# Performance work log

Measured on AMD Instinct MI355X. Metric: run time of the kernel, lower is better.

Reference implementation:

```python
import jax, jax.numpy as jnp
import numpy as np
import math

B_, L_, H_, N_ = 4, 4096, 512, 128

def setup_inputs() -> dict:
    key = jax.random.key(0)
    ks = jax.random.split(key, 6)
    return {
        "x": jax.random.normal(ks[0], (B_, L_, H_), dtype=jnp.float32),
        "log_Lam_real": jnp.log(0.5 * jnp.ones((N_,), jnp.float32)),  # log(-lam_real), lam_real=-0.5
        "Lam_imag": math.pi * jnp.arange(N_, dtype=jnp.float32),
        "B_real": jax.random.normal(ks[1], (N_, H_), jnp.float32) * 0.02,
        "B_imag": jax.random.normal(ks[2], (N_, H_), jnp.float32) * 0.02,
        "C_real": jax.random.normal(ks[3], (H_, N_), jnp.float32) * 0.02,
        "C_imag": jax.random.normal(ks[4], (H_, N_), jnp.float32) * 0.02,
        "D": jnp.ones((H_,), jnp.float32),
        "log_dt": jnp.zeros((1,), jnp.float32),
        "W_out": jax.random.normal(ks[5], (H_, H_), jnp.float32) * (1.0 / math.sqrt(H_)),
        "b_out": jnp.zeros((H_,), jnp.float32),
    }

def reference(x, log_Lam_real, Lam_imag, B_real, B_imag, C_real, C_imag, D, log_dt, W_out, b_out):
    B, L, H = x.shape
    N = log_Lam_real.shape[0]
    dt = jnp.exp(log_dt)                      # (1,)
    Lam_r = -jnp.exp(log_Lam_real)            # (N,)
    decay = jnp.exp(Lam_r * dt)               # (N,)
    Lbar_r = decay * jnp.cos(Lam_imag * dt)   # (N,)
    Lbar_i = decay * jnp.sin(Lam_imag * dt)   # (N,)
    # Precompute input projections for all timesteps: u @ (dt*B).T -> (B, L, N)
    Bu_r = dt * jnp.einsum('blh,nh->bln', x, B_real)
    Bu_i = dt * jnp.einsum('blh,nh->bln', x, B_imag)

    def step(carry, inp):
        sr, si = carry
        br, bi = inp
        sr_n = Lbar_r * sr - Lbar_i * si + br
        si_n = Lbar_r * si + Lbar_i * sr + bi
        return (sr_n, si_n), (sr_n, si_n)

    init = (jnp.zeros((B, N), x.dtype), jnp.zeros((B, N), x.dtype))
    (sr_f, si_f), (Sr, Si) = jax.lax.scan(
        step, init, (jnp.swapaxes(Bu_r, 0, 1), jnp.swapaxes(Bu_i, 0, 1)))
    Sr = jnp.swapaxes(Sr, 0, 1)  # (B, L, N)
    Si = jnp.swapaxes(Si, 0, 1)
    y = (jnp.einsum('bln,hn->blh', Sr, C_real)
         - jnp.einsum('bln,hn->blh', Si, C_imag)
         + D * x)
    out = y @ W_out.T + b_out  # dropout p=0 -> identity
    return out, (sr_f, si_f)
```

## Files before the change

kernel.cpp:

```cpp
#include <hip/hip_runtime.h>

typedef __attribute__((ext_vector_type(8))) short bf16x8;
typedef __attribute__((ext_vector_type(4))) float f32x4;

__device__ __forceinline__ unsigned short f2bf(float f) {
  unsigned u = __float_as_uint(f);
  return (unsigned short)((u + 0x7fffu + ((u >> 16) & 1u)) >> 16);
}
__device__ __forceinline__ float bf2f(unsigned short h) {
  return __uint_as_float(((unsigned)h) << 16);
}
__device__ __forceinline__ void gload_lds16(const void* g, void* l) {
  __builtin_amdgcn_global_load_lds((__attribute__((address_space(1))) void*)g,
                                   (__attribute__((address_space(3))) void*)l,
                                   16, 0, 0);
}
#define VMCNT(n) asm volatile("s_waitcnt vmcnt(" #n ")" ::: "memory")
#define LGKM0() asm volatile("s_waitcnt lgkmcnt(0)" ::: "memory")
#define SB0() __builtin_amdgcn_sched_barrier(0)
#define BAR() __builtin_amdgcn_s_barrier()

__global__ __launch_bounds__(256) void prepW1_k(
    const float* __restrict__ log_dt,
    const float* __restrict__ B_real, const float* __restrict__ B_imag,
    unsigned short* __restrict__ W1) {
  const float dtv = expf(log_dt[0]);
  const int i = blockIdx.x * 256 + threadIdx.x;
  const int j = i >> 9, h = i & 511;
  const float v = (j < 128) ? B_real[j * 512 + h] : B_imag[(j - 128) * 512 + h];
  W1[i] = f2bf(dtv * v);
}

__global__ __launch_bounds__(512, 1) void fused1_k(
    const float* __restrict__ x, const unsigned short* __restrict__ W1g,
    unsigned short* __restrict__ xbf, unsigned short* __restrict__ S2,
    const float* __restrict__ log_Lam_real, const float* __restrict__ Lam_imag,
    const float* __restrict__ log_dt, float* __restrict__ finals,
    const float* __restrict__ C_real, const float* __restrict__ C_imag,
    const float* __restrict__ W_out, const float* __restrict__ Dv,
    unsigned short* __restrict__ W45) {
  __shared__ unsigned short lds[61440];
  const int tid = threadIdx.x;
  const int bid = blockIdx.x;

  if (bid >= 256) {
    if (bid < 768) {
      const int i = (bid - 256) * 512 + tid;
      const int j = i >> 9, h = i & 511;
      W45[j * 768 + 256 + h] = f2bf(W_out[i] * Dv[h]);
    } else {
      float4* red = (float4*)lds;
      const int j0 = (bid - 768) * 2;
      const int kg = tid & 63;
      const int hc = tid >> 6;
      const int k4 = kg * 4;
      const bool im = (kg >= 32);
      const float* cbase = im ? (C_imag + (k4 - 128)) : (C_real + k4);
      const float* w0 = W_out + (long)j0 * 512;
      const float* w1 = w0 + 512;
      float4 acc0 = {0.f, 0.f, 0.f, 0.f}, acc1 = {0.f, 0.f, 0.f, 0.f};
#pragma unroll 8
      for (int hh = 0; hh < 64; ++hh) {
        const int h = hc * 64 + hh;
        const float4 cv = *(const float4*)(cbase + (long)h * 128);
        const float s0 = w0[h], s1 = w1[h];
        acc0.x += cv.x * s0; acc0.y += cv.y * s0; acc0.z += cv.z * s0; acc0.w += cv.w * s0;
        acc1.x += cv.x * s1; acc1.y += cv.y * s1; acc1.z += cv.z * s1; acc1.w += cv.w * s1;
      }
      if (im) {
        acc0.x = -acc0.x; acc0.y = -acc0.y; acc0.z = -acc0.z; acc0.w = -acc0.w;
        acc1.x = -acc1.x; acc1.y = -acc1.y; acc1.z = -acc1.z; acc1.w = -acc1.w;
      }
      red[(hc * 2 + 0) * 64 + kg] = acc0;
      red[(hc * 2 + 1) * 64 + kg] = acc1;
      __syncthreads();
      if (tid < 128) {
        const int r = tid >> 6, g = tid & 63;
        float4 s = {0.f, 0.f, 0.f, 0.f};
#pragma unroll
        for (int h8 = 0; h8 < 8; ++h8) {
          const float4 t = red[(h8 * 2 + r) * 64 + g];
          s.x += t.x; s.y += t.y; s.z += t.z; s.w += t.w;
        }
        unsigned short* o = W45 + (long)(j0 + r) * 768 + g * 4;
        o[0] = f2bf(s.x); o[1] = f2bf(s.y); o[2] = f2bf(s.z); o[3] = f2bf(s.w);
      }
    }
    return;
  }

  const int c = (bid & 7) * 32 + (bid >> 3);
  const int b = c >> 6, cb = c & 63;
  const int warm = cb ? 32 : 0;
  const long base = (long)b * 4096 + (long)cb * 64 - warm;

  const float dtv = expf(log_dt[0]);
  const int nidx = tid & 127;
  const float lamr = -expf(log_Lam_real[nidx]);
  const float dec = expf(lamr * dtv);
  const float th = Lam_imag[nidx] * dtv;
  const float Lr = dec * cosf(th);
  const float Li = dec * sinf(th);

  const int arow = tid >> 4;
  const int cg = tid & 15;
  const int wid_ = tid >> 6, lane_ = tid & 63;

  float4 a0S0, a1S0, a2S0, a0S1, a1S1, a2S1, a0S2, a1S2, a2S2;

#define LOADA(S, kt) {                                                   \
    const float* xp = x + base * 512 + (kt) * 64 + cg * 4;               \
    a0##S = *(const float4*)(xp + (long)arow * 512);                     \
    a1##S = *(const float4*)(xp + (long)(arow + 32) * 512);              \
    a2##S = *(const float4*)(xp + (long)(arow + 64) * 512); }

#define WRA1(V, R, buf, kt, DOX) {                                       \
    ushort4 hh_; hh_.x = f2bf(V.x); hh_.y = f2bf(V.y);                   \
    hh_.z = f2bf(V.z); hh_.w = f2bf(V.w);                                \
    const int seg_ = (cg >> 1) ^ ((R) & 7);                              \
    *(ushort4*)((char*)lds + (buf) * 12288 + (R) * 128 + seg_ * 16 +     \
                (cg & 1) * 8) = hh_;                                     \
    if (DOX) *(ushort4*)(xbf + (base + (R)) * 512 + (kt) * 64 + cg * 4) = hh_; }

#define WRITEA(S, buf, kt) {                                             \
    WRA1(a0##S, arow, buf, kt, (warm == 0));                             \
    WRA1(a1##S, arow + 32, buf, kt, 1);                                  \
    WRA1(a2##S, arow + 64, buf, kt, 1); }

  auto stageW = [&](int buf, int kt) {
#pragma unroll
    for (int i = 0; i < 4; ++i) {
      const int q = i * 8 + wid_;
      const int r = q * 8 + (lane_ >> 3);
      const int sg = lane_ & 7;
      gload_lds16(W1g + (long)r * 512 + kt * 64 + ((sg ^ (r & 7)) << 3),
                  lds + 12288 + buf * 16384 + q * 512 + lane_ * 8);
    }
  };

  const int wm = (wid_ >> 2) * 48;
  const int wn = (wid_ & 3) * 64;
  const int lrow = lane_ & 15, lgrp = lane_ >> 4;

  f32x4 acc[3][4];
#pragma unroll
  for (int mi = 0; mi < 3; ++mi)
#pragma unroll
    for (int ni = 0; ni < 4; ++ni) acc[mi][ni] = (f32x4){0.f, 0.f, 0.f, 0.f};

  auto mfma_step = [&](int abuf, int wbuf) {
    const unsigned short* As = lds + abuf * 6144;
    const unsigned short* Ws = lds + 12288 + wbuf * 16384;
#pragma unroll
    for (int kk = 0; kk < 2; ++kk) {
      bf16x8 af[3], wf[4];
#pragma unroll
      for (int mi = 0; mi < 3; ++mi) {
        const int r = wm + mi * 16 + lrow;
        af[mi] = *(const bf16x8*)(As + r * 64 + (((kk * 4 + lgrp) ^ (r & 7)) << 3));
      }
#pragma unroll
      for (int ni = 0; ni < 4; ++ni) {
        const int r = wn + ni * 16 + lrow;
        wf[ni] = *(const bf16x8*)(Ws + r * 64 + (((kk * 4 + lgrp) ^ (r & 7)) << 3));
      }
#pragma unroll
      for (int mi = 0; mi < 3; ++mi)
#pragma unroll
        for (int ni = 0; ni < 4; ++ni)
          acc[mi][ni] = __builtin_amdgcn_mfma_f32_16x16x32_bf16(af[mi], wf[ni],
                                                                acc[mi][ni], 0, 0, 0);
    }
  };

  LOADA(S0, 0);
  stageW(0, 0);
  VMCNT(4);
  WRITEA(S0, 0, 0);
  LOADA(S1, 1);
  stageW(1, 1);
  LOADA(S2, 2);
  VMCNT(7);
  LGKM0();
  SB0(); BAR(); SB0();

#pragma unroll
  for (int kt = 0; kt < 8; ++kt) {
    if (kt < 7) {
      if (((kt + 1) % 3) == 0) { WRITEA(S0, (kt + 1) & 1, kt + 1); }
      else if (((kt + 1) % 3) == 1) { WRITEA(S1, (kt + 1) & 1, kt + 1); }
      else { WRITEA(S2, (kt + 1) & 1, kt + 1); }
    }
    if (kt < 6) stageW((kt + 2) % 3, kt + 2);
    if (kt < 5) {
      if ((kt % 3) == 0) { LOADA(S0, kt + 3); }
      else if ((kt % 3) == 1) { LOADA(S1, kt + 3); }
      else { LOADA(S2, kt + 3); }
    }
    mfma_step(kt & 1, kt % 3);
    if (kt < 5) { VMCNT(7); }
    else if (kt == 5) { VMCNT(4); }
    else if (kt == 6) { VMCNT(0); }
    if (kt < 7) { LGKM0(); SB0(); BAR(); SB0(); }
  }
  __syncthreads();

#pragma unroll
  for (int mi = 0; mi < 3; ++mi)
#pragma unroll
    for (int ni = 0; ni < 4; ++ni)
#pragma unroll
      for (int e = 0; e < 4; ++e) {
        const int row = wm + mi * 16 + lgrp * 4 + e;
        const int col = wn + ni * 16 + lrow;
        lds[row * 256 + col] = f2bf(acc[mi][ni][e]);
      }
  __syncthreads();

  if (tid < 128) {
    float sr = 0.f, si = 0.f;
    for (int i = 0; i < warm; ++i) {
      const float br = bf2f(lds[i * 256 + tid]);
      const float bi = bf2f(lds[i * 256 + 128 + tid]);
      const float nr = Lr * sr - Li * si + br;
      const float ni_ = Lr * si + Li * sr + bi;
      sr = nr; si = ni_;
    }
    const long orow0 = (long)b * 4096 + cb * 64;
#pragma unroll 4
    for (int i = 0; i < 64; ++i) {
      const int li = warm + i;
      const float br = bf2f(lds[li * 256 + tid]);
      const float bi = bf2f(lds[li * 256 + 128 + tid]);
      const float nr = Lr * sr - Li * si + br;
      const float ni_ = Lr * si + Li * sr + bi;
      sr = nr; si = ni_;
      unsigned short* o = S2 + (orow0 + i) * 256;
      o[tid] = f2bf(sr);
      o[128 + tid] = f2bf(si);
    }
    if (cb == 63) {
      finals[b * 128 + tid] = sr;
      finals[512 + b * 128 + tid] = si;
    }
  }
#undef LOADA
#undef WRA1
#undef WRITEA
}

__global__ __launch_bounds__(256, 2) void gemm23_k(
    const unsigned short* __restrict__ S2, const unsigned short* __restrict__ xbf,
    const unsigned short* __restrict__ W45, float* __restrict__ out,
    const float* __restrict__ b_out) {
  constexpr int KT = 12;
  __shared__ unsigned short lds[2 * 16384];
  const int tid = threadIdx.x;
  const int id = blockIdx.x;
  const int swz = (id & 7) * 64 + (id >> 3);
  const int m0 = (swz >> 2) * 128;
  const int j0 = (swz & 3) * 128;

  const int r_ = tid >> 3;
  const int sg = tid & 7;

  auto stage = [&](int buf, int kt) {
    const unsigned short* asrc;
    long astr;
    int acol;
    if (kt < 4) { asrc = S2; astr = 256; acol = kt * 64; }
    else        { asrc = xbf; astr = 512; acol = (kt - 4) * 64; }
#pragma unroll
    for (int i = 0; i < 4; ++i) {
      const int r = i * 32 + r_;
      const int sp = sg ^ (r & 7);
      gload_lds16(asrc + (long)(m0 + r) * astr + acol + sp * 8,
                  lds + buf * 16384 + i * 2048 + tid * 8);
      gload_lds16(W45 + (long)(j0 + r) * 768 + kt * 64 + sp * 8,
                  lds + buf * 16384 + 8192 + i * 2048 + tid * 8);
    }
  };

  const int lane = tid & 63;
  const int wid = tid >> 6;
  const int wm = (wid >> 1) * 64;
  const int wn = (wid & 1) * 64;
  const int lrow = lane & 15;
  const int lgrp = lane >> 4;

  f32x4 acc[4][4];
#pragma unroll
  for (int mi = 0; mi < 4; ++mi)
#pragma unroll
    for (int ni = 0; ni < 4; ++ni) acc[mi][ni] = (f32x4){0.f, 0.f, 0.f, 0.f};

  stage(0, 0);
  int buf = 0;
#pragma unroll
  for (int kt = 0; kt < KT; ++kt) {
    VMCNT(0);
    SB0(); BAR(); SB0();
    if (kt + 1 < KT) stage(buf ^ 1, kt + 1);
    const unsigned short* As = lds + buf * 16384;
    const unsigned short* Ws = As + 8192;
#pragma unroll
    for (int kk = 0; kk < 2; ++kk) {
      bf16x8 af[4], wf[4];
#pragma unroll
      for (int mi = 0; mi < 4; ++mi) {
        const int r = wm + mi * 16 + lrow;
        af[mi] = *(const bf16x8*)(As + r * 64 + (((kk * 4 + lgrp) ^ (r & 7)) << 3));
      }
#pragma unroll
      for (int ni = 0; ni < 4; ++ni) {
        const int r = wn + ni * 16 + lrow;
        wf[ni] = *(const bf16x8*)(Ws + r * 64 + (((kk * 4 + lgrp) ^ (r & 7)) << 3));
      }
#pragma unroll
      for (int mi = 0; mi < 4; ++mi)
#pragma unroll
        for (int ni = 0; ni < 4; ++ni)
          acc[mi][ni] = __builtin_amdgcn_mfma_f32_16x16x32_bf16(af[mi], wf[ni],
                                                                acc[mi][ni], 0, 0, 0);
    }
    buf ^= 1;
  }

#pragma unroll
  for (int mi = 0; mi < 4; ++mi) {
#pragma unroll
    for (int ni = 0; ni < 4; ++ni) {
      const int row = m0 + wm + mi * 16 + lgrp * 4;
      const int col = j0 + wn + ni * 16 + lrow;
      const float bo = b_out[col];
      f32x4 v = acc[mi][ni];
#pragma unroll
      for (int e = 0; e < 4; ++e) out[(long)(row + e) * 512 + col] = v[e] + bo;
    }
  }
}

extern "C" void kernel_launch(void* const* d_in, const int* in_sizes, int n_in,
                              void* d_out, int out_size, void* d_ws, size_t ws_size,
                              hipStream_t stream) {
  const float* x      = (const float*)d_in[0];
  const float* logLr  = (const float*)d_in[1];
  const float* LamI   = (const float*)d_in[2];
  const float* B_real = (const float*)d_in[3];
  const float* B_imag = (const float*)d_in[4];
  const float* C_real = (const float*)d_in[5];
  const float* C_imag = (const float*)d_in[6];
  const float* Dv     = (const float*)d_in[7];
  const float* log_dt = (const float*)d_in[8];
  const float* W_out  = (const float*)d_in[9];
  const float* b_out  = (const float*)d_in[10];

  unsigned short* x_bf = (unsigned short*)d_ws;
  unsigned short* S2   = x_bf + 8388608;
  unsigned short* W1   = S2 + 4194304;
  unsigned short* W45  = W1 + 131072;

  float* out = (float*)d_out;
  float* finals = out + 8388608;

  prepW1_k<<<512, 256, 0, stream>>>(log_dt, B_real, B_imag, W1);
  fused1_k<<<1024, 512, 0, stream>>>(x, W1, x_bf, S2, logLr, LamI, log_dt, finals,
                                     C_real, C_imag, W_out, Dv, W45);
  gemm23_k<<<512, 256, 0, stream>>>(S2, x_bf, W45, out, b_out);
}
```

Baseline: 51.47 us.

## Merge scan and output GEMM into one cooperative kernel with grid sync

Replaces the two-kernel sequence (the fused projection+scan kernel and a separate output GEMM) with a single cooperative launch of 256 blocks. W45 preparation moves onto the otherwise idle threads (128..511) of the scan blocks, and a grid-wide sync then separates it from a second phase in which each block computes two 128x128 output tiles using a 3-stage global-to-LDS pipeline. This removes one kernel launch boundary and the separate small blocks. In exchange the GEMM runs on only 256 blocks with one block per CU, and the grid sync adds its own cost.

```diff
diff --git a/kernel.cpp b/kernel.cpp
--- a/kernel.cpp
+++ b/kernel.cpp
@@ -1,4 +1,7 @@
 #include <hip/hip_runtime.h>
+#include <hip/hip_cooperative_groups.h>
+
+namespace cg = cooperative_groups;
 
 typedef __attribute__((ext_vector_type(8))) short bf16x8;
 typedef __attribute__((ext_vector_type(4))) float f32x4;
@@ -31,63 +34,18 @@
   W1[i] = f2bf(dtv * v);
 }
 
-__global__ __launch_bounds__(512, 1) void fused1_k(
+__global__ __launch_bounds__(512, 1) void coop_k(
     const float* __restrict__ x, const unsigned short* __restrict__ W1g,
     unsigned short* __restrict__ xbf, unsigned short* __restrict__ S2,
     const float* __restrict__ log_Lam_real, const float* __restrict__ Lam_imag,
     const float* __restrict__ log_dt, float* __restrict__ finals,
     const float* __restrict__ C_real, const float* __restrict__ C_imag,
     const float* __restrict__ W_out, const float* __restrict__ Dv,
-    unsigned short* __restrict__ W45) {
+    unsigned short* __restrict__ W45, float* __restrict__ out,
+    const float* __restrict__ b_out) {
   __shared__ unsigned short lds[61440];
   const int tid = threadIdx.x;
   const int bid = blockIdx.x;
-
-  if (bid >= 256) {
-    if (bid < 768) {
-      const int i = (bid - 256) * 512 + tid;
-      const int j = i >> 9, h = i & 511;
-      W45[j * 768 + 256 + h] = f2bf(W_out[i] * Dv[h]);
-    } else {
-      float4* red = (float4*)lds;
-      const int j0 = (bid - 768) * 2;
-      const int kg = tid & 63;
-      const int hc = tid >> 6;
-      const int k4 = kg * 4;
-      const bool im = (kg >= 32);
-      const float* cbase = im ? (C_imag + (k4 - 128)) : (C_real + k4);
-      const float* w0 = W_out + (long)j0 * 512;
-      const float* w1 = w0 + 512;
-      float4 acc0 = {0.f, 0.f, 0.f, 0.f}, acc1 = {0.f, 0.f, 0.f, 0.f};
-#pragma unroll 8
-      for (int hh = 0; hh < 64; ++hh) {
-        const int h = hc * 64 + hh;
-        const float4 cv = *(const float4*)(cbase + (long)h * 128);
-        const float s0 = w0[h], s1 = w1[h];
-        acc0.x += cv.x * s0; acc0.y += cv.y * s0; acc0.z += cv.z * s0; acc0.w += cv.w * s0;
-        acc1.x += cv.x * s1; acc1.y += cv.y * s1; acc1.z += cv.z * s1; acc1.w += cv.w * s1;
-      }
-      if (im) {
-        acc0.x = -acc0.x; acc0.y = -acc0.y; acc0.z = -acc0.z; acc0.w = -acc0.w;
-        acc1.x = -acc1.x; acc1.y = -acc1.y; acc1.z = -acc1.z; acc1.w = -acc1.w;
-      }
-      red[(hc * 2 + 0) * 64 + kg] = acc0;
-      red[(hc * 2 + 1) * 64 + kg] = acc1;
-      __syncthreads();
-      if (tid < 128) {
-        const int r = tid >> 6, g = tid & 63;
-        float4 s = {0.f, 0.f, 0.f, 0.f};
-#pragma unroll
-        for (int h8 = 0; h8 < 8; ++h8) {
-          const float4 t = red[(h8 * 2 + r) * 64 + g];
-          s.x += t.x; s.y += t.y; s.z += t.z; s.w += t.w;
-        }
-        unsigned short* o = W45 + (long)(j0 + r) * 768 + g * 4;
-        o[0] = f2bf(s.x); o[1] = f2bf(s.y); o[2] = f2bf(s.z); o[3] = f2bf(s.w);
-      }
-    }
-    return;
-  }
 
   const int c = (bid & 7) * 32 + (bid >> 3);
   const int b = c >> 6, cb = c & 63;
@@ -103,13 +61,13 @@
   const float Li = dec * sinf(th);
 
   const int arow = tid >> 4;
-  const int cg = tid & 15;
+  const int cg2 = tid & 15;
   const int wid_ = tid >> 6, lane_ = tid & 63;
 
   float4 a0S0, a1S0, a2S0, a0S1, a1S1, a2S1, a0S2, a1S2, a2S2;
 
 #define LOADA(S, kt) {                                                   \
-    const float* xp = x + base * 512 + (kt) * 64 + cg * 4;               \
+    const float* xp = x + base * 512 + (kt) * 64 + cg2 * 4;              \
     a0##S = *(const float4*)(xp + (long)arow * 512);                     \
     a1##S = *(const float4*)(xp + (long)(arow + 32) * 512);              \
     a2##S = *(const float4*)(xp + (long)(arow + 64) * 512); }
@@ -117,10 +75,10 @@
 #define WRA1(V, R, buf, kt, DOX) {                                       \
     ushort4 hh_; hh_.x = f2bf(V.x); hh_.y = f2bf(V.y);                   \
     hh_.z = f2bf(V.z); hh_.w = f2bf(V.w);                                \
-    const int seg_ = (cg >> 1) ^ ((R) & 7);                              \
+    const int seg_ = (cg2 >> 1) ^ ((R) & 7);                             \
     *(ushort4*)((char*)lds + (buf) * 12288 + (R) * 128 + seg_ * 16 +     \
-                (cg & 1) * 8) = hh_;                                     \
-    if (DOX) *(ushort4*)(xbf + (base + (R)) * 512 + (kt) * 64 + cg * 4) = hh_; }
+                (cg2 & 1) * 8) = hh_;                                    \
+    if (DOX) *(ushort4*)(xbf + (base + (R)) * 512 + (kt) * 64 + cg2 * 4) = hh_; }
 
 #define WRITEA(S, buf, kt) {                                             \
     WRA1(a0##S, arow, buf, kt, (warm == 0));                             \
@@ -243,101 +201,145 @@
       finals[b * 128 + tid] = sr;
       finals[512 + b * 128 + tid] = si;
     }
+  } else if (tid < 256) {
+    const int t5 = tid - 128;
+#pragma unroll
+    for (int e = 0; e < 8; ++e) {
+      const int i = bid * 1024 + e * 128 + t5;
+      const int j = i >> 9, h = i & 511;
+      W45[j * 768 + 256 + h] = f2bf(W_out[i] * Dv[h]);
+    }
+  } else {
+    float4* red = (float4*)(lds + 24576);
+    const int t2 = tid - 256;
+    const int kg = t2 & 63, hc = t2 >> 6;
+    const int k4 = kg * 4;
+    const bool im = (kg >= 32);
+    const float* cbase = im ? (C_imag + (k4 - 128)) : (C_real + k4);
+    const int j0 = bid * 2;
+    const float* w0 = W_out + (long)j0 * 512;
+    const float* w1 = w0 + 512;
+    float4 acc0 = {0.f, 0.f, 0.f, 0.f}, acc1 = {0.f, 0.f, 0.f, 0.f};
+#pragma unroll 8
+    for (int hh = 0; hh < 128; ++hh) {
+      const int h = hc * 128 + hh;
+      const float4 cv = *(const float4*)(cbase + (long)h * 128);
+      const float s0 = w0[h], s1 = w1[h];
+      acc0.x += cv.x * s0; acc0.y += cv.y * s0; acc0.z += cv.z * s0; acc0.w += cv.w * s0;
+      acc1.x += cv.x * s1; acc1.y += cv.y * s1; acc1.z += cv.z * s1; acc1.w += cv.w * s1;
+    }
+    if (im) {
+      acc0.x = -acc0.x; acc0.y = -acc0.y; acc0.z = -acc0.z; acc0.w = -acc0.w;
+      acc1.x = -acc1.x; acc1.y = -acc1.y; acc1.z = -acc1.z; acc1.w = -acc1.w;
+    }
+    red[(hc * 2 + 0) * 64 + kg] = acc0;
+    red[(hc * 2 + 1) * 64 + kg] = acc1;
+  }
+  __syncthreads();
+  if (tid >= 256 && tid < 384) {
+    float4* red = (float4*)(lds + 24576);
+    const int t2 = tid - 256;
+    const int r = t2 >> 6, g = t2 & 63;
+    float4 s = {0.f, 0.f, 0.f, 0.f};
+#pragma unroll
+    for (int h4 = 0; h4 < 4; ++h4) {
+      const float4 t = red[(h4 * 2 + r) * 64 + g];
+      s.x += t.x; s.y += t.y; s.z += t.z; s.w += t.w;
+    }
+    unsigned short* o = W45 + (long)(bid * 2 + r) * 768 + g * 4;
+    o[0] = f2bf(s.x); o[1] = f2bf(s.y); o[2] = f2bf(s.z); o[3] = f2bf(s.w);
+  }
+
+  cg::this_grid().sync();
+
+  {
+    const int xcd = bid & 7, l = bid >> 3;
+    const int m0 = ((xcd << 4) + (l >> 1)) * 128;
+    const int r8b = tid >> 3;
+    const int sgb = tid & 7;
+
+    auto stage2 = [&](int buf, int kt, int j0) {
+      const unsigned short* asrc;
+      long astr;
+      int acol;
+      if (kt < 4) { asrc = S2; astr = 256; acol = kt * 64; }
+      else        { asrc = xbf; astr = 512; acol = (kt - 4) * 64; }
+#pragma unroll
+      for (int i = 0; i < 2; ++i) {
+        const int r = i * 64 + r8b;
+        const int sp = sgb ^ (r & 7);
+        gload_lds16(asrc + (long)(m0 + r) * astr + acol + sp * 8,
+                    lds + buf * 16384 + i * 4096 + tid * 8);
+        gload_lds16(W45 + (long)(j0 + r) * 768 + kt * 64 + sp * 8,
+                    lds + buf * 16384 + 8192 + i * 4096 + tid * 8);
+      }
+    };
+
+    const int wm2 = (wid_ >> 2) * 64;
+    const int wn2 = (wid_ & 3) * 32;
+
+#pragma unroll
+    for (int t = 0; t < 2; ++t) {
+      const int j0 = (((l & 1) << 1) + t) * 128;
+      f32x4 acc2[4][2];
+#pragma unroll
+      for (int mi = 0; mi < 4; ++mi)
+#pragma unroll
+        for (int ni = 0; ni < 2; ++ni) acc2[mi][ni] = (f32x4){0.f, 0.f, 0.f, 0.f};
+
+      __syncthreads();
+      stage2(0, 0, j0);
+      stage2(1, 1, j0);
+      VMCNT(4);
+      SB0(); BAR(); SB0();
+
+#pragma unroll
+      for (int kt = 0; kt < 12; ++kt) {
+        if (kt + 2 < 12) stage2((kt + 2) % 3, kt + 2, j0);
+        const unsigned short* As = lds + (kt % 3) * 16384;
+        const unsigned short* Ws = As + 8192;
+#pragma unroll
+        for (int kk = 0; kk < 2; ++kk) {
+          bf16x8 af2[4], wf2[2];
+#pragma unroll
+          for (int mi = 0; mi < 4; ++mi) {
+            const int r = wm2 + mi * 16 + lrow;
+            af2[mi] = *(const bf16x8*)(As + r * 64 + (((kk * 4 + lgrp) ^ (r & 7)) << 3));
+          }
+#pragma unroll
+          for (int ni = 0; ni < 2; ++ni) {
+            const int r = wn2 + ni * 16 + lrow;
+            wf2[ni] = *(const bf16x8*)(Ws + r * 64 + (((kk * 4 + lgrp) ^ (r & 7)) << 3));
+          }
+#pragma unroll
+          for (int mi = 0; mi < 4; ++mi)
+#pragma unroll
+            for (int ni = 0; ni < 2; ++ni)
+              acc2[mi][ni] = __builtin_amdgcn_mfma_f32_16x16x32_bf16(
+                  af2[mi], wf2[ni], acc2[mi][ni], 0, 0, 0);
+        }
+        if (kt + 2 < 12) { VMCNT(4); }
+        else if (kt == 10) { VMCNT(0); }
+        if (kt < 11) { SB0(); BAR(); SB0(); }
+      }
+
+#pragma unroll
+      for (int mi = 0; mi < 4; ++mi) {
+#pragma unroll
+        for (int ni = 0; ni < 2; ++ni) {
+          const int row = m0 + wm2 + mi * 16 + lgrp * 4;
+          const int col = j0 + wn2 + ni * 16 + lrow;
+          const float bo = b_out[col];
+          f32x4 v = acc2[mi][ni];
+#pragma unroll
+          for (int e = 0; e < 4; ++e) out[(long)(row + e) * 512 + col] = v[e] + bo;
+        }
+      }
+    }
   }
 #undef LOADA
 #undef WRA1
 #undef WRITEA
-}
-
-__global__ __launch_bounds__(256, 2) void gemm23_k(
-    const unsigned short* __restrict__ S2, const unsigned short* __restrict__ xbf,
-    const unsigned short* __restrict__ W45, float* __restrict__ out,
-    const float* __restrict__ b_out) {
-  constexpr int KT = 12;
-  __shared__ unsigned short lds[2 * 16384];
-  const int tid = threadIdx.x;
-  const int id = blockIdx.x;
-  const int swz = (id & 7) * 64 + (id >> 3);
-  const int m0 = (swz >> 2) * 128;
-  const int j0 = (swz & 3) * 128;
-
-  const int r_ = tid >> 3;
-  const int sg = tid & 7;
-
-  auto stage = [&](int buf, int kt) {
-    const unsigned short* asrc;
-    long astr;
-    int acol;
-    if (kt < 4) { asrc = S2; astr = 256; acol = kt * 64; }
-    else        { asrc = xbf; astr = 512; acol = (kt - 4) * 64; }
-#pragma unroll
-    for (int i = 0; i < 4; ++i) {
-      const int r = i * 32 + r_;
-      const int sp = sg ^ (r & 7);
-      gload_lds16(asrc + (long)(m0 + r) * astr + acol + sp * 8,
-                  lds + buf * 16384 + i * 2048 + tid * 8);
-      gload_lds16(W45 + (long)(j0 + r) * 768 + kt * 64 + sp * 8,
-                  lds + buf * 16384 + 8192 + i * 2048 + tid * 8);
-    }
-  };
-
-  const int lane = tid & 63;
-  const int wid = tid >> 6;
-  const int wm = (wid >> 1) * 64;
-  const int wn = (wid & 1) * 64;
-  const int lrow = lane & 15;
-  const int lgrp = lane >> 4;
-
-  f32x4 acc[4][4];
-#pragma unroll
-  for (int mi = 0; mi < 4; ++mi)
-#pragma unroll
-    for (int ni = 0; ni < 4; ++ni) acc[mi][ni] = (f32x4){0.f, 0.f, 0.f, 0.f};
-
-  stage(0, 0);
-  int buf = 0;
-#pragma unroll
-  for (int kt = 0; kt < KT; ++kt) {
-    VMCNT(0);
-    SB0(); BAR(); SB0();
-    if (kt + 1 < KT) stage(buf ^ 1, kt + 1);
-    const unsigned short* As = lds + buf * 16384;
-    const unsigned short* Ws = As + 8192;
-#pragma unroll
-    for (int kk = 0; kk < 2; ++kk) {
-      bf16x8 af[4], wf[4];
-#pragma unroll
-      for (int mi = 0; mi < 4; ++mi) {
-        const int r = wm + mi * 16 + lrow;
-        af[mi] = *(const bf16x8*)(As + r * 64 + (((kk * 4 + lgrp) ^ (r & 7)) << 3));
-      }
-#pragma unroll
-      for (int ni = 0; ni < 4; ++ni) {
-        const int r = wn + ni * 16 + lrow;
-        wf[ni] = *(const bf16x8*)(Ws + r * 64 + (((kk * 4 + lgrp) ^ (r & 7)) << 3));
-      }
-#pragma unroll
-      for (int mi = 0; mi < 4; ++mi)
-#pragma unroll
-        for (int ni = 0; ni < 4; ++ni)
-          acc[mi][ni] = __builtin_amdgcn_mfma_f32_16x16x32_bf16(af[mi], wf[ni],
-                                                                acc[mi][ni], 0, 0, 0);
-    }
-    buf ^= 1;
-  }
-
-#pragma unroll
-  for (int mi = 0; mi < 4; ++mi) {
-#pragma unroll
-    for (int ni = 0; ni < 4; ++ni) {
-      const int row = m0 + wm + mi * 16 + lgrp * 4;
-      const int col = j0 + wn + ni * 16 + lrow;
-      const float bo = b_out[col];
-      f32x4 v = acc[mi][ni];
-#pragma unroll
-      for (int e = 0; e < 4; ++e) out[(long)(row + e) * 512 + col] = v[e] + bo;
-    }
-  }
 }
 
 extern "C" void kernel_launch(void* const* d_in, const int* in_sizes, int n_in,
@@ -364,7 +366,10 @@
   float* finals = out + 8388608;
 
   prepW1_k<<<512, 256, 0, stream>>>(log_dt, B_real, B_imag, W1);
-  fused1_k<<<1024, 512, 0, stream>>>(x, W1, x_bf, S2, logLr, LamI, log_dt, finals,
-                                     C_real, C_imag, W_out, Dv, W45);
-  gemm23_k<<<512, 256, 0, stream>>>(S2, x_bf, W45, out, b_out);
-}
+
+  void* args[] = {(void*)&x,      (void*)&W1,     (void*)&x_bf,  (void*)&S2,
+                  (void*)&logLr,  (void*)&LamI,   (void*)&log_dt, (void*)&finals,
+                  (void*)&C_real, (void*)&C_imag, (void*)&W_out,  (void*)&Dv,
+                  (void*)&W45,    (void*)&out,    (void*)&b_out};
+  hipLaunchCooperativeKernel((void*)coop_k, dim3(256), dim3(512), args, 0, stream);
+}
```

New measurement: 84.80 us. +64.7%, slower.
